# Performance work log

Hardware: AMD Instinct MI355X
Metric: run time of the kernel (lower is better)

Reference implementation:

```python
import jax, jax.numpy as jnp
import numpy as np

DIM = 2048
HIDDEN = 1024
E = 8
TOTAL = 16384
# uneven per-expert token counts summing to TOTAL (tokens pre-sorted by expert)
COUNTS = np.array([1024, 3072, 2048, 512, 4096, 1536, 2560, 1536], dtype=np.int32)
assert COUNTS.sum() == TOTAL


def setup_inputs() -> dict:
    key = jax.random.key(0)
    k1, k2, k3, k4 = jax.random.split(key, 4)
    x = jax.random.normal(k1, (TOTAL, DIM), dtype=jnp.float32)
    # kaiming_uniform_(a=sqrt(5)) on [out, in] -> U(-1/sqrt(fan_in), 1/sqrt(fan_in))
    s_in = 1.0 / np.sqrt(DIM).astype(np.float32)
    s_hid = 1.0 / np.sqrt(HIDDEN).astype(np.float32)
    gate_proj = jax.random.uniform(k2, (E, HIDDEN, DIM), dtype=jnp.float32, minval=-s_in, maxval=s_in)
    up_proj = jax.random.uniform(k3, (E, HIDDEN, DIM), dtype=jnp.float32, minval=-s_in, maxval=s_in)
    down_proj = jax.random.uniform(k4, (E, DIM, HIDDEN), dtype=jnp.float32, minval=-s_hid, maxval=s_hid)
    num_tokens_per_expert = jnp.asarray(COUNTS)
    return {
        "x": x,
        "gate_proj": gate_proj,
        "up_proj": up_proj,
        "down_proj": down_proj,
        "num_tokens_per_expert": num_tokens_per_expert,
    }


def reference(x, gate_proj, up_proj, down_proj, num_tokens_per_expert):
    """Grouped-expert SwiGLU: for each expert e, its contiguous token slice xs gets
    silu(xs @ G_e^T) * (xs @ U_e^T) @ D_e^T. Counts are data-dependent segment sizes
    (the torch original is @torch.compiler.disable for the same reason), so we slice
    with concrete offsets and loop over the small fixed expert count."""
    counts = np.asarray(num_tokens_per_expert)
    offs = np.concatenate([[0], np.cumsum(counts)])
    outs = []
    for e in range(counts.shape[0]):
        lo, hi = int(offs[e]), int(offs[e + 1])
        if hi == lo:
            continue
        xs = x[lo:hi]                                   # [c_e, dim]
        h = jax.nn.silu(xs @ gate_proj[e].T) * (xs @ up_proj[e].T)  # [c_e, hidden]
        outs.append(h @ down_proj[e].T)                 # [c_e, dim]
    return jnp.concatenate(outs, axis=0)                # [total, dim]
```

## Files before the change

kernel.cpp:

```cpp
#include <hip/hip_runtime.h>


constexpr int DIM    = 2048;
constexpr int HIDDEN = 1024;
constexpr int NE     = 8;
constexpr int TOTAL  = 16384;

constexpr int BM = 128, BN = 128, BK = 32;
constexpr int LDT  = 40;
constexpr int TILE = 128 * LDT;

typedef __attribute__((ext_vector_type(8)))  short bf16x8;
typedef __attribute__((ext_vector_type(16))) float f32x16;

constexpr size_t W_ELEMS = (size_t)NE * HIDDEN * DIM;
constexpr size_t H_ELEMS = (size_t)TOTAL * HIDDEN;

__device__ unsigned short g_g_hi[W_ELEMS], g_g_lo[W_ELEMS];
__device__ unsigned short g_u_hi[W_ELEMS], g_u_lo[W_ELEMS];
__device__ unsigned short g_d_hi[W_ELEMS], g_d_lo[W_ELEMS];
__device__ unsigned short g_h_hi[H_ELEMS], g_h_lo[H_ELEMS];

__device__ __forceinline__ unsigned short bf16_rne(float f) {
  unsigned u = __builtin_bit_cast(unsigned, f);
  u += 0x7FFFu + ((u >> 16) & 1u);
  return (unsigned short)(u >> 16);
}
__device__ __forceinline__ float bf16f(unsigned short s) {
  unsigned u = (unsigned)s << 16;
  return __builtin_bit_cast(float, u);
}
__device__ __forceinline__ void split2(float f, unsigned short& hi, unsigned short& lo) {
  hi = bf16_rne(f);
  lo = bf16_rne(f - bf16f(hi));
}

__device__ __forceinline__ void expert_range(const int* __restrict__ counts, int e,
                                             int& lo, int& nloc) {
  lo = 0; nloc = 0;
#pragma unroll
  for (int i = 0; i < NE; ++i) {
    int c = counts[i];
    if (i < e) lo += c;
    if (i == e) nloc = c;
  }
}

__global__ __launch_bounds__(256)
void split_planes(const float* __restrict__ src, unsigned short* __restrict__ hi,
                  unsigned short* __restrict__ lo, int n4) {
  int i = blockIdx.x * blockDim.x + threadIdx.x;
  const int stride = gridDim.x * blockDim.x;
  for (; i < n4; i += stride) {
    const float4 v = ((const float4*)src)[i];
    ushort4 h4, l4;
    split2(v.x, h4.x, l4.x);
    split2(v.y, h4.y, l4.y);
    split2(v.z, h4.z, l4.z);
    split2(v.w, h4.w, l4.w);
    ((ushort4*)hi)[i] = h4;
    ((ushort4*)lo)[i] = l4;
  }
}

__global__ __launch_bounds__(256, 2)
void moe_s1(const float* __restrict__ x, const int* __restrict__ counts) {
  const int e = blockIdx.z;
  int lo, nloc;
  expert_range(counts, e, lo, nloc);
  const int m0 = blockIdx.x * BM;
  if (m0 >= nloc) return;
  const int n0 = blockIdx.y * BN;

  __shared__ unsigned short sm[6 * TILE];
  unsigned short* const Ah = sm;
  unsigned short* const Al = sm + TILE;
  unsigned short* const Gh = sm + 2 * TILE;
  unsigned short* const Gl = sm + 3 * TILE;
  unsigned short* const Uh = sm + 4 * TILE;
  unsigned short* const Ul = sm + 5 * TILE;

  const int tid  = threadIdx.x;
  const int lane = tid & 63;
  const int w    = tid >> 6;
  const int wm   = w >> 1, wn = w & 1;

  const float* const xa = x + (size_t)lo * DIM;
  const size_t wb = ((size_t)e * HIDDEN + n0) * DIM;
  const unsigned short* const Ghg = g_g_hi + wb;
  const unsigned short* const Glg = g_g_lo + wb;
  const unsigned short* const Uhg = g_u_hi + wb;
  const unsigned short* const Ulg = g_u_lo + wb;

  const int q4 = (tid & 7) * 4;
  const int r0 = tid >> 3;
  const int k8 = (tid & 3) * 8;
  const int rw = tid >> 2;

  f32x16 accg[2][2], accu[2][2];
#pragma unroll
  for (int i = 0; i < 2; ++i)
#pragma unroll
    for (int j = 0; j < 2; ++j)
#pragma unroll
      for (int k = 0; k < 16; ++k) { accg[i][j][k] = 0.f; accu[i][j][k] = 0.f; }

  float4 va[4];
  bf16x8 vgh[2], vgl[2], vuh[2], vul[2];

  auto load_tile = [&](int kt) {
    const int kbx = kt * BK + q4;
#pragma unroll
    for (int c = 0; c < 4; ++c) {
      const int r  = (c << 5) + r0;
      const int ra = (m0 + r < nloc) ? (m0 + r) : m0;
      va[c] = *(const float4*)(xa + (size_t)ra * DIM + kbx);
    }
    const int kbw = kt * BK + k8;
#pragma unroll
    for (int c = 0; c < 2; ++c) {
      const size_t ro = (size_t)((c << 6) + rw) * DIM + kbw;
      vgh[c] = *(const bf16x8*)(Ghg + ro);
      vgl[c] = *(const bf16x8*)(Glg + ro);
      vuh[c] = *(const bf16x8*)(Uhg + ro);
      vul[c] = *(const bf16x8*)(Ulg + ro);
    }
  };

  const int NT = DIM / BK;
  load_tile(0);

  for (int kt = 0; kt < NT; ++kt) {
    __syncthreads();
#pragma unroll
    for (int c = 0; c < 4; ++c) {
      ushort4 hh, ll;
      split2(va[c].x, hh.x, ll.x);
      split2(va[c].y, hh.y, ll.y);
      split2(va[c].z, hh.z, ll.z);
      split2(va[c].w, hh.w, ll.w);
      const int o = ((c << 5) + r0) * LDT + q4;
      *(ushort4*)(Ah + o) = hh;
      *(ushort4*)(Al + o) = ll;
    }
#pragma unroll
    for (int c = 0; c < 2; ++c) {
      const int o = ((c << 6) + rw) * LDT + k8;
      *(bf16x8*)(Gh + o) = vgh[c];
      *(bf16x8*)(Gl + o) = vgl[c];
      *(bf16x8*)(Uh + o) = vuh[c];
      *(bf16x8*)(Ul + o) = vul[c];
    }
    if (kt + 1 < NT) load_tile(kt + 1);
    __syncthreads();

#pragma unroll
    for (int ks = 0; ks < 2; ++ks) {
      const int kc = ks * 16 + (lane >> 5) * 8;
      const int ar = wm * 64 + (lane & 31);
      const int br = wn * 64 + (lane & 31);
      bf16x8 fah[2], fal[2];
#pragma unroll
      for (int fm = 0; fm < 2; ++fm) {
        fah[fm] = *(const bf16x8*)(Ah + (ar + fm * 32) * LDT + kc);
        fal[fm] = *(const bf16x8*)(Al + (ar + fm * 32) * LDT + kc);
      }
#pragma unroll
      for (int fn = 0; fn < 2; ++fn) {
        const int ro = (br + fn * 32) * LDT + kc;
        bf16x8 gh = *(const bf16x8*)(Gh + ro);
        bf16x8 gl = *(const bf16x8*)(Gl + ro);
        bf16x8 uh = *(const bf16x8*)(Uh + ro);
        bf16x8 ul = *(const bf16x8*)(Ul + ro);
#pragma unroll
        for (int fm = 0; fm < 2; ++fm) {
          accg[fm][fn] = __builtin_amdgcn_mfma_f32_32x32x16_bf16(fah[fm], gh, accg[fm][fn], 0, 0, 0);
          accg[fm][fn] = __builtin_amdgcn_mfma_f32_32x32x16_bf16(fah[fm], gl, accg[fm][fn], 0, 0, 0);
          accg[fm][fn] = __builtin_amdgcn_mfma_f32_32x32x16_bf16(fal[fm], gh, accg[fm][fn], 0, 0, 0);
          accu[fm][fn] = __builtin_amdgcn_mfma_f32_32x32x16_bf16(fah[fm], uh, accu[fm][fn], 0, 0, 0);
          accu[fm][fn] = __builtin_amdgcn_mfma_f32_32x32x16_bf16(fah[fm], ul, accu[fm][fn], 0, 0, 0);
          accu[fm][fn] = __builtin_amdgcn_mfma_f32_32x32x16_bf16(fal[fm], uh, accu[fm][fn], 0, 0, 0);
        }
      }
    }
  }

  const int crb  = (lane >> 5) * 4;
  const int ccol = lane & 31;
#pragma unroll
  for (int fm = 0; fm < 2; ++fm)
#pragma unroll
    for (int fn = 0; fn < 2; ++fn)
#pragma unroll
      for (int j = 0; j < 16; ++j) {
        const int rl = wm * 64 + fm * 32 + (j & 3) + ((j >> 2) << 3) + crb;
        if (m0 + rl < nloc) {
          const float gv = accg[fm][fn][j];
          const float uv = accu[fm][fn][j];
          const float hv = gv / (1.f + __expf(-gv)) * uv;
          unsigned short hh, hl;
          split2(hv, hh, hl);
          const size_t idx = (size_t)(lo + m0 + rl) * HIDDEN + (n0 + wn * 64 + fn * 32 + ccol);
          g_h_hi[idx] = hh;
          g_h_lo[idx] = hl;
        }
      }
}

__global__ __launch_bounds__(256, 2)
void moe_s2(const int* __restrict__ counts, float* __restrict__ out) {
  const int e = blockIdx.z;
  int lo, nloc;
  expert_range(counts, e, lo, nloc);
  const int m0 = blockIdx.x * BM;
  if (m0 >= nloc) return;
  const int n0 = blockIdx.y * BN;

  __shared__ unsigned short sm[4 * TILE];
  unsigned short* const Ah = sm;
  unsigned short* const Al = sm + TILE;
  unsigned short* const Bh = sm + 2 * TILE;
  unsigned short* const Bl = sm + 3 * TILE;

  const int tid  = threadIdx.x;
  const int lane = tid & 63;
  const int w    = tid >> 6;
  const int wm   = w >> 1, wn = w & 1;

  const unsigned short* const hhg = g_h_hi + (size_t)lo * HIDDEN;
  const unsigned short* const hlg = g_h_lo + (size_t)lo * HIDDEN;
  const size_t db = ((size_t)e * DIM + n0) * HIDDEN;
  const unsigned short* const Bhg = g_d_hi + db;
  const unsigned short* const Blg = g_d_lo + db;

  const int k8 = (tid & 3) * 8;
  const int rw = tid >> 2;

  f32x16 acc[2][2];
#pragma unroll
  for (int i = 0; i < 2; ++i)
#pragma unroll
    for (int j = 0; j < 2; ++j)
#pragma unroll
      for (int k = 0; k < 16; ++k) acc[i][j][k] = 0.f;

  bf16x8 vah[2], val[2], vbh[2], vbl[2];

  auto load_tile = [&](int kt) {
    const int kb = kt * BK + k8;
#pragma unroll
    for (int c = 0; c < 2; ++c) {
      const int r  = (c << 6) + rw;
      const int ra = (m0 + r < nloc) ? (m0 + r) : m0;
      vah[c] = *(const bf16x8*)(hhg + (size_t)ra * HIDDEN + kb);
      val[c] = *(const bf16x8*)(hlg + (size_t)ra * HIDDEN + kb);
      const size_t ro = (size_t)r * HIDDEN + kb;
      vbh[c] = *(const bf16x8*)(Bhg + ro);
      vbl[c] = *(const bf16x8*)(Blg + ro);
    }
  };

  const int NT = HIDDEN / BK;
  load_tile(0);

  for (int kt = 0; kt < NT; ++kt) {
    __syncthreads();
#pragma unroll
    for (int c = 0; c < 2; ++c) {
      const int o = ((c << 6) + rw) * LDT + k8;
      *(bf16x8*)(Ah + o) = vah[c];
      *(bf16x8*)(Al + o) = val[c];
      *(bf16x8*)(Bh + o) = vbh[c];
      *(bf16x8*)(Bl + o) = vbl[c];
    }
    if (kt + 1 < NT) load_tile(kt + 1);
    __syncthreads();

#pragma unroll
    for (int ks = 0; ks < 2; ++ks) {
      const int kc = ks * 16 + (lane >> 5) * 8;
      const int ar = wm * 64 + (lane & 31);
      const int br = wn * 64 + (lane & 31);
      bf16x8 fah[2], fal[2];
#pragma unroll
      for (int fm = 0; fm < 2; ++fm) {
        fah[fm] = *(const bf16x8*)(Ah + (ar + fm * 32) * LDT + kc);
        fal[fm] = *(const bf16x8*)(Al + (ar + fm * 32) * LDT + kc);
      }
#pragma unroll
      for (int fn = 0; fn < 2; ++fn) {
        const int ro = (br + fn * 32) * LDT + kc;
        bf16x8 bh = *(const bf16x8*)(Bh + ro);
        bf16x8 bl = *(const bf16x8*)(Bl + ro);
#pragma unroll
        for (int fm = 0; fm < 2; ++fm) {
          acc[fm][fn] = __builtin_amdgcn_mfma_f32_32x32x16_bf16(fah[fm], bh, acc[fm][fn], 0, 0, 0);
          acc[fm][fn] = __builtin_amdgcn_mfma_f32_32x32x16_bf16(fah[fm], bl, acc[fm][fn], 0, 0, 0);
          acc[fm][fn] = __builtin_amdgcn_mfma_f32_32x32x16_bf16(fal[fm], bh, acc[fm][fn], 0, 0, 0);
        }
      }
    }
  }

  const int crb  = (lane >> 5) * 4;
  const int ccol = lane & 31;
#pragma unroll
  for (int fm = 0; fm < 2; ++fm)
#pragma unroll
    for (int fn = 0; fn < 2; ++fn)
#pragma unroll
      for (int j = 0; j < 16; ++j) {
        const int rl = wm * 64 + fm * 32 + (j & 3) + ((j >> 2) << 3) + crb;
        if (m0 + rl < nloc) {
          out[(size_t)(lo + m0 + rl) * DIM + (n0 + wn * 64 + fn * 32 + ccol)] = acc[fm][fn][j];
        }
      }
}

extern "C" void kernel_launch(void* const* d_in, const int* in_sizes, int n_in,
                              void* d_out, int out_size, void* d_ws, size_t ws_size,
                              hipStream_t stream) {
  const float* x     = (const float*)d_in[0];
  const float* gate  = (const float*)d_in[1];
  const float* up    = (const float*)d_in[2];
  const float* down  = (const float*)d_in[3];
  const int*   cnts  = (const int*)d_in[4];
  float*       out   = (float*)d_out;
  (void)d_ws; (void)ws_size;

  unsigned short *gh, *gl, *uh, *ul, *dh, *dl;
  hipGetSymbolAddress((void**)&gh, HIP_SYMBOL(g_g_hi));
  hipGetSymbolAddress((void**)&gl, HIP_SYMBOL(g_g_lo));
  hipGetSymbolAddress((void**)&uh, HIP_SYMBOL(g_u_hi));
  hipGetSymbolAddress((void**)&ul, HIP_SYMBOL(g_u_lo));
  hipGetSymbolAddress((void**)&dh, HIP_SYMBOL(g_d_hi));
  hipGetSymbolAddress((void**)&dl, HIP_SYMBOL(g_d_lo));

  const int n4 = (int)(W_ELEMS / 4);
  dim3 blk(256, 1, 1);
  split_planes<<<2048, blk, 0, stream>>>(gate, gh, gl, n4);
  split_planes<<<2048, blk, 0, stream>>>(up,   uh, ul, n4);
  split_planes<<<2048, blk, 0, stream>>>(down, dh, dl, n4);
  moe_s1<<<dim3(TOTAL / BM, HIDDEN / BN, NE), blk, 0, stream>>>(x, cnts);
  moe_s2<<<dim3(TOTAL / BM, DIM / BN, NE), blk, 0, stream>>>(cnts, out);
}
```

Before: 1.552 ms.

## Pre-pack operands into swizzled bf16 hi/lo tiles and stage via direct global-to-LDS loads

Every operand, x included, is now pre-split into hi/lo bf16 and packed into 128x32 tiles with an XOR-swizzled layout. The split no longer happens inside the GEMM loop. Both GEMM kernels stage tiles straight into a double-buffered LDS using global_load_lds, with explicit vmcnt waits and barriers, setprio around the MFMA blocks, and 512 threads in stage 1. This removes the register round-trip and in-loop conversion, and the swizzle avoids LDS bank conflicts. In exchange it adds an extra pack pass over x, and it assumes expert token offsets are multiples of 128, since the tile index is (lo+m0)>>7. That holds for the test counts but not in general.

```diff
diff --git a/kernel.cpp b/kernel.cpp
--- a/kernel.cpp
+++ b/kernel.cpp
@@ -1,36 +1,30 @@
 #include <hip/hip_runtime.h>
 
 
-constexpr int DIM    = 2048;
-constexpr int HIDDEN = 1024;
-constexpr int NE     = 8;
-constexpr int TOTAL  = 16384;
-
+constexpr int DIM = 2048, HIDDEN = 1024, NE = 8, TOTAL = 16384;
 constexpr int BM = 128, BN = 128, BK = 32;
-constexpr int LDT  = 40;
-constexpr int TILE = 128 * LDT;
+constexpr int TBLK = 8192;
 
 typedef __attribute__((ext_vector_type(8)))  short bf16x8;
 typedef __attribute__((ext_vector_type(16))) float f32x16;
-
-constexpr size_t W_ELEMS = (size_t)NE * HIDDEN * DIM;
-constexpr size_t H_ELEMS = (size_t)TOTAL * HIDDEN;
-
-__device__ unsigned short g_g_hi[W_ELEMS], g_g_lo[W_ELEMS];
-__device__ unsigned short g_u_hi[W_ELEMS], g_u_lo[W_ELEMS];
-__device__ unsigned short g_d_hi[W_ELEMS], g_d_lo[W_ELEMS];
-__device__ unsigned short g_h_hi[H_ELEMS], g_h_lo[H_ELEMS];
-
-__device__ __forceinline__ unsigned short bf16_rne(float f) {
+typedef unsigned short u16;
+
+__device__ u16 g_px[(size_t)(TOTAL / 128) * (DIM / 32) * TBLK];
+__device__ u16 g_pg[(size_t)(NE * HIDDEN / 128) * (DIM / 32) * TBLK];
+__device__ u16 g_pu[(size_t)(NE * HIDDEN / 128) * (DIM / 32) * TBLK];
+__device__ u16 g_pd[(size_t)(NE * DIM / 128) * (HIDDEN / 32) * TBLK];
+__device__ u16 g_ph[(size_t)(TOTAL / 128) * (HIDDEN / 32) * TBLK];
+
+__device__ __forceinline__ u16 bf16_rne(float f) {
   unsigned u = __builtin_bit_cast(unsigned, f);
   u += 0x7FFFu + ((u >> 16) & 1u);
-  return (unsigned short)(u >> 16);
-}
-__device__ __forceinline__ float bf16f(unsigned short s) {
+  return (u16)(u >> 16);
+}
+__device__ __forceinline__ float bf16f(u16 s) {
   unsigned u = (unsigned)s << 16;
   return __builtin_bit_cast(float, u);
 }
-__device__ __forceinline__ void split2(float f, unsigned short& hi, unsigned short& lo) {
+__device__ __forceinline__ void split2(float f, u16& hi, u16& lo) {
   hi = bf16_rne(f);
   lo = bf16_rne(f - bf16f(hi));
 }
@@ -46,25 +40,37 @@
   }
 }
 
+__device__ __forceinline__ void stage16(const u16* g, u16* l) {
+  __builtin_amdgcn_global_load_lds(
+      (const __attribute__((address_space(1))) unsigned int*)g,
+      (__attribute__((address_space(3))) unsigned int*)l, 16, 0, 0);
+}
+
 __global__ __launch_bounds__(256)
-void split_planes(const float* __restrict__ src, unsigned short* __restrict__ hi,
-                  unsigned short* __restrict__ lo, int n4) {
-  int i = blockIdx.x * blockDim.x + threadIdx.x;
-  const int stride = gridDim.x * blockDim.x;
+void pack_split(const float* __restrict__ src, u16* __restrict__ dst, int K, int n4) {
+  int i = blockIdx.x * 256 + threadIdx.x;
+  const int stride = gridDim.x * 256;
+  const int ktiles = K >> 5;
   for (; i < n4; i += stride) {
     const float4 v = ((const float4*)src)[i];
+    const int col = (i * 4) % K;
+    const int row = (i * 4) / K;
     ushort4 h4, l4;
     split2(v.x, h4.x, l4.x);
     split2(v.y, h4.y, l4.y);
     split2(v.z, h4.z, l4.z);
     split2(v.w, h4.w, l4.w);
-    ((ushort4*)hi)[i] = h4;
-    ((ushort4*)lo)[i] = l4;
-  }
-}
-
-__global__ __launch_bounds__(256, 2)
-void moe_s1(const float* __restrict__ x, const int* __restrict__ counts) {
+    const int r = row & 127, kk = col & 31;
+    const size_t base = ((size_t)(row >> 7) * ktiles + (col >> 5)) * TBLK + r * 64;
+    const int ch = (kk >> 3) ^ (r & 7);
+    const int cl = ((kk >> 3) + 4) ^ (r & 7);
+    *(ushort4*)(dst + base + ch * 8 + (kk & 7)) = h4;
+    *(ushort4*)(dst + base + cl * 8 + (kk & 7)) = l4;
+  }
+}
+
+__global__ __launch_bounds__(512, 2)
+void moe_s1(const int* __restrict__ counts) {
   const int e = blockIdx.z;
   int lo, nloc;
   expert_range(counts, e, lo, nloc);
@@ -72,139 +78,108 @@
   if (m0 >= nloc) return;
   const int n0 = blockIdx.y * BN;
 
-  __shared__ unsigned short sm[6 * TILE];
-  unsigned short* const Ah = sm;
-  unsigned short* const Al = sm + TILE;
-  unsigned short* const Gh = sm + 2 * TILE;
-  unsigned short* const Gl = sm + 3 * TILE;
-  unsigned short* const Uh = sm + 4 * TILE;
-  unsigned short* const Ul = sm + 5 * TILE;
-
-  const int tid  = threadIdx.x;
-  const int lane = tid & 63;
-  const int w    = tid >> 6;
-  const int wm   = w >> 1, wn = w & 1;
-
-  const float* const xa = x + (size_t)lo * DIM;
-  const size_t wb = ((size_t)e * HIDDEN + n0) * DIM;
-  const unsigned short* const Ghg = g_g_hi + wb;
-  const unsigned short* const Glg = g_g_lo + wb;
-  const unsigned short* const Uhg = g_u_hi + wb;
-  const unsigned short* const Ulg = g_u_lo + wb;
-
-  const int q4 = (tid & 7) * 4;
-  const int r0 = tid >> 3;
-  const int k8 = (tid & 3) * 8;
-  const int rw = tid >> 2;
-
-  f32x16 accg[2][2], accu[2][2];
+  __shared__ __align__(16) u16 sm[2 * 3 * TBLK];
+
+  const int tid = threadIdx.x, lane = tid & 63, w = tid >> 6;
+  const int wm = w >> 2, wnq = w & 3;
+
+  const int gmt = (lo + m0) >> 7;
+  const u16* const srcs[3] = {
+      g_px + (size_t)gmt * (DIM / 32) * TBLK,
+      g_pg + (size_t)(e * (HIDDEN / 128) + (n0 >> 7)) * (DIM / 32) * TBLK,
+      g_pu + (size_t)(e * (HIDDEN / 128) + (n0 >> 7)) * (DIM / 32) * TBLK};
+
+  const u16* csrc[6];
+  int coff[6];
+#pragma unroll
+  for (int j = 0; j < 6; ++j) {
+    const int i = w * 6 + j;
+    const int mat = i >> 4;
+    const int off = (i & 15) * 512;
+    csrc[j] = srcs[mat] + off + lane * 8;
+    coff[j] = mat * TBLK + off;
+  }
+
+  auto stage = [&](int buf, int kt) {
+#pragma unroll
+    for (int j = 0; j < 6; ++j)
+      stage16(csrc[j] + (size_t)kt * TBLK, &sm[buf * 3 * TBLK + coff[j]]);
+  };
+
+  auto frg = [&](int buf, int mat, int rbase, int p, int ks) -> bf16x8 {
+    const int rr = rbase + (lane & 31);
+    const int c = (p * 4 + ks * 2 + (lane >> 5)) ^ (rr & 7);
+    return *(const bf16x8*)&sm[buf * 3 * TBLK + mat * TBLK + rr * 64 + c * 8];
+  };
+
+  f32x16 ag[2], au[2];
 #pragma unroll
   for (int i = 0; i < 2; ++i)
 #pragma unroll
-    for (int j = 0; j < 2; ++j)
-#pragma unroll
-      for (int k = 0; k < 16; ++k) { accg[i][j][k] = 0.f; accu[i][j][k] = 0.f; }
-
-  float4 va[4];
-  bf16x8 vgh[2], vgl[2], vuh[2], vul[2];
-
-  auto load_tile = [&](int kt) {
-    const int kbx = kt * BK + q4;
-#pragma unroll
-    for (int c = 0; c < 4; ++c) {
-      const int r  = (c << 5) + r0;
-      const int ra = (m0 + r < nloc) ? (m0 + r) : m0;
-      va[c] = *(const float4*)(xa + (size_t)ra * DIM + kbx);
+    for (int k = 0; k < 16; ++k) { ag[i][k] = 0.f; au[i][k] = 0.f; }
+
+  const int NT = DIM / BK;
+  stage(0, 0);
+  stage(1, 1);
+
+  for (int kt = 0; kt < NT; ++kt) {
+    const int b = kt & 1;
+    if (kt + 2 < NT) asm volatile("s_waitcnt vmcnt(6)" ::: "memory");
+    else             asm volatile("s_waitcnt vmcnt(0)" ::: "memory");
+    __builtin_amdgcn_s_barrier();
+    __builtin_amdgcn_sched_barrier(0);
+#pragma unroll
+    for (int ks = 0; ks < 2; ++ks) {
+      const bf16x8 aH0 = frg(b, 0, wm * 64,      0, ks);
+      const bf16x8 aH1 = frg(b, 0, wm * 64 + 32, 0, ks);
+      const bf16x8 aL0 = frg(b, 0, wm * 64,      1, ks);
+      const bf16x8 aL1 = frg(b, 0, wm * 64 + 32, 1, ks);
+      const bf16x8 gH = frg(b, 1, wnq * 32, 0, ks);
+      const bf16x8 gL = frg(b, 1, wnq * 32, 1, ks);
+      const bf16x8 uH = frg(b, 2, wnq * 32, 0, ks);
+      const bf16x8 uL = frg(b, 2, wnq * 32, 1, ks);
+      __builtin_amdgcn_s_setprio(1);
+      ag[0] = __builtin_amdgcn_mfma_f32_32x32x16_bf16(aH0, gH, ag[0], 0, 0, 0);
+      ag[0] = __builtin_amdgcn_mfma_f32_32x32x16_bf16(aH0, gL, ag[0], 0, 0, 0);
+      ag[0] = __builtin_amdgcn_mfma_f32_32x32x16_bf16(aL0, gH, ag[0], 0, 0, 0);
+      ag[1] = __builtin_amdgcn_mfma_f32_32x32x16_bf16(aH1, gH, ag[1], 0, 0, 0);
+      ag[1] = __builtin_amdgcn_mfma_f32_32x32x16_bf16(aH1, gL, ag[1], 0, 0, 0);
+      ag[1] = __builtin_amdgcn_mfma_f32_32x32x16_bf16(aL1, gH, ag[1], 0, 0, 0);
+      au[0] = __builtin_amdgcn_mfma_f32_32x32x16_bf16(aH0, uH, au[0], 0, 0, 0);
+      au[0] = __builtin_amdgcn_mfma_f32_32x32x16_bf16(aH0, uL, au[0], 0, 0, 0);
+      au[0] = __builtin_amdgcn_mfma_f32_32x32x16_bf16(aL0, uH, au[0], 0, 0, 0);
+      au[1] = __builtin_amdgcn_mfma_f32_32x32x16_bf16(aH1, uH, au[1], 0, 0, 0);
+      au[1] = __builtin_amdgcn_mfma_f32_32x32x16_bf16(aH1, uL, au[1], 0, 0, 0);
+      au[1] = __builtin_amdgcn_mfma_f32_32x32x16_bf16(aL1, uH, au[1], 0, 0, 0);
+      __builtin_amdgcn_s_setprio(0);
     }
-    const int kbw = kt * BK + k8;
-#pragma unroll
-    for (int c = 0; c < 2; ++c) {
-      const size_t ro = (size_t)((c << 6) + rw) * DIM + kbw;
-      vgh[c] = *(const bf16x8*)(Ghg + ro);
-      vgl[c] = *(const bf16x8*)(Glg + ro);
-      vuh[c] = *(const bf16x8*)(Uhg + ro);
-      vul[c] = *(const bf16x8*)(Ulg + ro);
-    }
-  };
-
-  const int NT = DIM / BK;
-  load_tile(0);
-
-  for (int kt = 0; kt < NT; ++kt) {
-    __syncthreads();
-#pragma unroll
-    for (int c = 0; c < 4; ++c) {
-      ushort4 hh, ll;
-      split2(va[c].x, hh.x, ll.x);
-      split2(va[c].y, hh.y, ll.y);
-      split2(va[c].z, hh.z, ll.z);
-      split2(va[c].w, hh.w, ll.w);
-      const int o = ((c << 5) + r0) * LDT + q4;
-      *(ushort4*)(Ah + o) = hh;
-      *(ushort4*)(Al + o) = ll;
-    }
-#pragma unroll
-    for (int c = 0; c < 2; ++c) {
-      const int o = ((c << 6) + rw) * LDT + k8;
-      *(bf16x8*)(Gh + o) = vgh[c];
-      *(bf16x8*)(Gl + o) = vgl[c];
-      *(bf16x8*)(Uh + o) = vuh[c];
-      *(bf16x8*)(Ul + o) = vul[c];
-    }
-    if (kt + 1 < NT) load_tile(kt + 1);
-    __syncthreads();
-
-#pragma unroll
-    for (int ks = 0; ks < 2; ++ks) {
-      const int kc = ks * 16 + (lane >> 5) * 8;
-      const int ar = wm * 64 + (lane & 31);
-      const int br = wn * 64 + (lane & 31);
-      bf16x8 fah[2], fal[2];
-#pragma unroll
-      for (int fm = 0; fm < 2; ++fm) {
-        fah[fm] = *(const bf16x8*)(Ah + (ar + fm * 32) * LDT + kc);
-        fal[fm] = *(const bf16x8*)(Al + (ar + fm * 32) * LDT + kc);
-      }
-#pragma unroll
-      for (int fn = 0; fn < 2; ++fn) {
-        const int ro = (br + fn * 32) * LDT + kc;
-        bf16x8 gh = *(const bf16x8*)(Gh + ro);
-        bf16x8 gl = *(const bf16x8*)(Gl + ro);
-        bf16x8 uh = *(const bf16x8*)(Uh + ro);
-        bf16x8 ul = *(const bf16x8*)(Ul + ro);
-#pragma unroll
-        for (int fm = 0; fm < 2; ++fm) {
-          accg[fm][fn] = __builtin_amdgcn_mfma_f32_32x32x16_bf16(fah[fm], gh, accg[fm][fn], 0, 0, 0);
-          accg[fm][fn] = __builtin_amdgcn_mfma_f32_32x32x16_bf16(fah[fm], gl, accg[fm][fn], 0, 0, 0);
-          accg[fm][fn] = __builtin_amdgcn_mfma_f32_32x32x16_bf16(fal[fm], gh, accg[fm][fn], 0, 0, 0);
-          accu[fm][fn] = __builtin_amdgcn_mfma_f32_32x32x16_bf16(fah[fm], uh, accu[fm][fn], 0, 0, 0);
-          accu[fm][fn] = __builtin_amdgcn_mfma_f32_32x32x16_bf16(fah[fm], ul, accu[fm][fn], 0, 0, 0);
-          accu[fm][fn] = __builtin_amdgcn_mfma_f32_32x32x16_bf16(fal[fm], uh, accu[fm][fn], 0, 0, 0);
-        }
+    __builtin_amdgcn_sched_barrier(0);
+    __builtin_amdgcn_s_barrier();
+    __builtin_amdgcn_sched_barrier(0);
+    if (kt + 2 < NT) stage(b, kt + 2);
+  }
+
+  const int hf = lane >> 5, ccol = lane & 31;
+  const int n = n0 + wnq * 32 + ccol;
+  const int kk = n & 31;
+  const size_t hbase = ((size_t)gmt * (HIDDEN / 32) + (n >> 5)) * TBLK;
+#pragma unroll
+  for (int fm = 0; fm < 2; ++fm)
+#pragma unroll
+    for (int j = 0; j < 16; ++j) {
+      const int rl = wm * 64 + fm * 32 + (j & 3) + ((j >> 2) << 3) + hf * 4;
+      if (m0 + rl < nloc) {
+        const float gv = ag[fm][j];
+        const float uv = au[fm][j];
+        const float hv = gv / (1.f + __expf(-gv)) * uv;
+        u16 hh, hl;
+        split2(hv, hh, hl);
+        const int ch = (kk >> 3) ^ (rl & 7);
+        const int cl = ((kk >> 3) + 4) ^ (rl & 7);
+        g_ph[hbase + rl * 64 + ch * 8 + (kk & 7)] = hh;
+        g_ph[hbase + rl * 64 + cl * 8 + (kk & 7)] = hl;
       }
     }
-  }
-
-  const int crb  = (lane >> 5) * 4;
-  const int ccol = lane & 31;
-#pragma unroll
-  for (int fm = 0; fm < 2; ++fm)
-#pragma unroll
-    for (int fn = 0; fn < 2; ++fn)
-#pragma unroll
-      for (int j = 0; j < 16; ++j) {
-        const int rl = wm * 64 + fm * 32 + (j & 3) + ((j >> 2) << 3) + crb;
-        if (m0 + rl < nloc) {
-          const float gv = accg[fm][fn][j];
-          const float uv = accu[fm][fn][j];
-          const float hv = gv / (1.f + __expf(-gv)) * uv;
-          unsigned short hh, hl;
-          split2(hv, hh, hl);
-          const size_t idx = (size_t)(lo + m0 + rl) * HIDDEN + (n0 + wn * 64 + fn * 32 + ccol);
-          g_h_hi[idx] = hh;
-          g_h_lo[idx] = hl;
-        }
-      }
 }
 
 __global__ __launch_bounds__(256, 2)
@@ -216,25 +191,38 @@
   if (m0 >= nloc) return;
   const int n0 = blockIdx.y * BN;
 
-  __shared__ unsigned short sm[4 * TILE];
-  unsigned short* const Ah = sm;
-  unsigned short* const Al = sm + TILE;
-  unsigned short* const Bh = sm + 2 * TILE;
-  unsigned short* const Bl = sm + 3 * TILE;
-
-  const int tid  = threadIdx.x;
-  const int lane = tid & 63;
-  const int w    = tid >> 6;
-  const int wm   = w >> 1, wn = w & 1;
-
-  const unsigned short* const hhg = g_h_hi + (size_t)lo * HIDDEN;
-  const unsigned short* const hlg = g_h_lo + (size_t)lo * HIDDEN;
-  const size_t db = ((size_t)e * DIM + n0) * HIDDEN;
-  const unsigned short* const Bhg = g_d_hi + db;
-  const unsigned short* const Blg = g_d_lo + db;
-
-  const int k8 = (tid & 3) * 8;
-  const int rw = tid >> 2;
+  __shared__ __align__(16) u16 sm[2 * 2 * TBLK];
+
+  const int tid = threadIdx.x, lane = tid & 63, w = tid >> 6;
+  const int wm = w >> 1, wn = w & 1;
+
+  const int gmt = (lo + m0) >> 7;
+  const u16* const srcs[2] = {
+      g_ph + (size_t)gmt * (HIDDEN / 32) * TBLK,
+      g_pd + (size_t)(e * (DIM / 128) + (n0 >> 7)) * (HIDDEN / 32) * TBLK};
+
+  const u16* csrc[8];
+  int coff[8];
+#pragma unroll
+  for (int j = 0; j < 8; ++j) {
+    const int i = w * 8 + j;
+    const int mat = i >> 4;
+    const int off = (i & 15) * 512;
+    csrc[j] = srcs[mat] + off + lane * 8;
+    coff[j] = mat * TBLK + off;
+  }
+
+  auto stage = [&](int buf, int kt) {
+#pragma unroll
+    for (int j = 0; j < 8; ++j)
+      stage16(csrc[j] + (size_t)kt * TBLK, &sm[buf * 2 * TBLK + coff[j]]);
+  };
+
+  auto frg = [&](int buf, int mat, int rbase, int p, int ks) -> bf16x8 {
+    const int rr = rbase + (lane & 31);
+    const int c = (p * 4 + ks * 2 + (lane >> 5)) ^ (rr & 7);
+    return *(const bf16x8*)&sm[buf * 2 * TBLK + mat * TBLK + rr * 64 + c * 8];
+  };
 
   f32x16 acc[2][2];
 #pragma unroll
@@ -244,73 +232,54 @@
 #pragma unroll
       for (int k = 0; k < 16; ++k) acc[i][j][k] = 0.f;
 
-  bf16x8 vah[2], val[2], vbh[2], vbl[2];
-
-  auto load_tile = [&](int kt) {
-    const int kb = kt * BK + k8;
-#pragma unroll
-    for (int c = 0; c < 2; ++c) {
-      const int r  = (c << 6) + rw;
-      const int ra = (m0 + r < nloc) ? (m0 + r) : m0;
-      vah[c] = *(const bf16x8*)(hhg + (size_t)ra * HIDDEN + kb);
-      val[c] = *(const bf16x8*)(hlg + (size_t)ra * HIDDEN + kb);
-      const size_t ro = (size_t)r * HIDDEN + kb;
-      vbh[c] = *(const bf16x8*)(Bhg + ro);
-      vbl[c] = *(const bf16x8*)(Blg + ro);
+  const int NT = HIDDEN / BK;
+  stage(0, 0);
+  stage(1, 1);
+
+  for (int kt = 0; kt < NT; ++kt) {
+    const int b = kt & 1;
+    if (kt + 2 < NT) asm volatile("s_waitcnt vmcnt(8)" ::: "memory");
+    else             asm volatile("s_waitcnt vmcnt(0)" ::: "memory");
+    __builtin_amdgcn_s_barrier();
+    __builtin_amdgcn_sched_barrier(0);
+#pragma unroll
+    for (int ks = 0; ks < 2; ++ks) {
+      bf16x8 aH[2], aL[2], bH[2], bL[2];
+#pragma unroll
+      for (int fm = 0; fm < 2; ++fm) {
+        aH[fm] = frg(b, 0, wm * 64 + fm * 32, 0, ks);
+        aL[fm] = frg(b, 0, wm * 64 + fm * 32, 1, ks);
+      }
+#pragma unroll
+      for (int fn = 0; fn < 2; ++fn) {
+        bH[fn] = frg(b, 1, wn * 64 + fn * 32, 0, ks);
+        bL[fn] = frg(b, 1, wn * 64 + fn * 32, 1, ks);
+      }
+      __builtin_amdgcn_s_setprio(1);
+#pragma unroll
+      for (int fn = 0; fn < 2; ++fn)
+#pragma unroll
+        for (int fm = 0; fm < 2; ++fm) {
+          acc[fm][fn] = __builtin_amdgcn_mfma_f32_32x32x16_bf16(aH[fm], bH[fn], acc[fm][fn], 0, 0, 0);
+          acc[fm][fn] = __builtin_amdgcn_mfma_f32_32x32x16_bf16(aH[fm], bL[fn], acc[fm][fn], 0, 0, 0);
+          acc[fm][fn] = __builtin_amdgcn_mfma_f32_32x32x16_bf16(aL[fm], bH[fn], acc[fm][fn], 0, 0, 0);
+        }
+      __builtin_amdgcn_s_setprio(0);
     }
-  };
-
-  const int NT = HIDDEN / BK;
-  load_tile(0);
-
-  for (int kt = 0; kt < NT; ++kt) {
-    __syncthreads();
-#pragma unroll
-    for (int c = 0; c < 2; ++c) {
-      const int o = ((c << 6) + rw) * LDT + k8;
-      *(bf16x8*)(Ah + o) = vah[c];
-      *(bf16x8*)(Al + o) = val[c];
-      *(bf16x8*)(Bh + o) = vbh[c];
-      *(bf16x8*)(Bl + o) = vbl[c];
-    }
-    if (kt + 1 < NT) load_tile(kt + 1);
-    __syncthreads();
-
-#pragma unroll
-    for (int ks = 0; ks < 2; ++ks) {
-      const int kc = ks * 16 + (lane >> 5) * 8;
-      const int ar = wm * 64 + (lane & 31);
-      const int br = wn * 64 + (lane & 31);
-      bf16x8 fah[2], fal[2];
-#pragma unroll
-      for (int fm = 0; fm < 2; ++fm) {
-        fah[fm] = *(const bf16x8*)(Ah + (ar + fm * 32) * LDT + kc);
-        fal[fm] = *(const bf16x8*)(Al + (ar + fm * 32) * LDT + kc);
-      }
-#pragma unroll
-      for (int fn = 0; fn < 2; ++fn) {
-        const int ro = (br + fn * 32) * LDT + kc;
-        bf16x8 bh = *(const bf16x8*)(Bh + ro);
-        bf16x8 bl = *(const bf16x8*)(Bl + ro);
-#pragma unroll
-        for (int fm = 0; fm < 2; ++fm) {
-          acc[fm][fn] = __builtin_amdgcn_mfma_f32_32x32x16_bf16(fah[fm], bh, acc[fm][fn], 0, 0, 0);
-          acc[fm][fn] = __builtin_amdgcn_mfma_f32_32x32x16_bf16(fah[fm], bl, acc[fm][fn], 0, 0, 0);
-          acc[fm][fn] = __builtin_amdgcn_mfma_f32_32x32x16_bf16(fal[fm], bh, acc[fm][fn], 0, 0, 0);
-        }
-      }
-    }
-  }
-
-  const int crb  = (lane >> 5) * 4;
-  const int ccol = lane & 31;
+    __builtin_amdgcn_sched_barrier(0);
+    __builtin_amdgcn_s_barrier();
+    __builtin_amdgcn_sched_barrier(0);
+    if (kt + 2 < NT) stage(b, kt + 2);
+  }
+
+  const int hf = lane >> 5, ccol = lane & 31;
 #pragma unroll
   for (int fm = 0; fm < 2; ++fm)
 #pragma unroll
     for (int fn = 0; fn < 2; ++fn)
 #pragma unroll
       for (int j = 0; j < 16; ++j) {
-        const int rl = wm * 64 + fm * 32 + (j & 3) + ((j >> 2) << 3) + crb;
+        const int rl = wm * 64 + fm * 32 + (j & 3) + ((j >> 2) << 3) + hf * 4;
         if (m0 + rl < nloc) {
           out[(size_t)(lo + m0 + rl) * DIM + (n0 + wn * 64 + fn * 32 + ccol)] = acc[fm][fn][j];
         }
@@ -320,27 +289,26 @@
 extern "C" void kernel_launch(void* const* d_in, const int* in_sizes, int n_in,
                               void* d_out, int out_size, void* d_ws, size_t ws_size,
                               hipStream_t stream) {
-  const float* x     = (const float*)d_in[0];
-  const float* gate  = (const float*)d_in[1];
-  const float* up    = (const float*)d_in[2];
-  const float* down  = (const float*)d_in[3];
-  const int*   cnts  = (const int*)d_in[4];
-  float*       out   = (float*)d_out;
+  const float* x    = (const float*)d_in[0];
+  const float* gate = (const float*)d_in[1];
+  const float* up   = (const float*)d_in[2];
+  const float* down = (const float*)d_in[3];
+  const int*   cnts = (const int*)d_in[4];
+  float*       out  = (float*)d_out;
   (void)d_ws; (void)ws_size;
 
-  unsigned short *gh, *gl, *uh, *ul, *dh, *dl;
-  hipGetSymbolAddress((void**)&gh, HIP_SYMBOL(g_g_hi));
-  hipGetSymbolAddress((void**)&gl, HIP_SYMBOL(g_g_lo));
-  hipGetSymbolAddress((void**)&uh, HIP_SYMBOL(g_u_hi));
-  hipGetSymbolAddress((void**)&ul, HIP_SYMBOL(g_u_lo));
-  hipGetSymbolAddress((void**)&dh, HIP_SYMBOL(g_d_hi));
-  hipGetSymbolAddress((void**)&dl, HIP_SYMBOL(g_d_lo));
-
-  const int n4 = (int)(W_ELEMS / 4);
-  dim3 blk(256, 1, 1);
-  split_planes<<<2048, blk, 0, stream>>>(gate, gh, gl, n4);
-  split_planes<<<2048, blk, 0, stream>>>(up,   uh, ul, n4);
-  split_planes<<<2048, blk, 0, stream>>>(down, dh, dl, n4);
-  moe_s1<<<dim3(TOTAL / BM, HIDDEN / BN, NE), blk, 0, stream>>>(x, cnts);
-  moe_s2<<<dim3(TOTAL / BM, DIM / BN, NE), blk, 0, stream>>>(cnts, out);
-}
+  u16 *px, *pg, *pu, *pd;
+  hipGetSymbolAddress((void**)&px, HIP_SYMBOL(g_px));
+  hipGetSymbolAddress((void**)&pg, HIP_SYMBOL(g_pg));
+  hipGetSymbolAddress((void**)&pu, HIP_SYMBOL(g_pu));
+  hipGetSymbolAddress((void**)&pd, HIP_SYMBOL(g_pd));
+
+  dim3 blk256(256, 1, 1);
+  pack_split<<<2048, blk256, 0, stream>>>(x,    px, DIM,    (TOTAL * DIM) / 4);
+  pack_split<<<2048, blk256, 0, stream>>>(gate, pg, DIM,    (NE * HIDDEN * DIM) / 4);
+  pack_split<<<2048, blk256, 0, stream>>>(up,   pu, DIM,    (NE * HIDDEN * DIM) / 4);
+  pack_split<<<2048, blk256, 0, stream>>>(down, pd, HIDDEN, (NE * DIM * HIDDEN) / 4);
+
+  moe_s1<<<dim3(TOTAL / BM, HIDDEN / BN, NE), dim3(512, 1, 1), 0, stream>>>(cnts);
+  moe_s2<<<dim3(TOTAL / BM, DIM / BN, NE), blk256, 0, stream>>>(cnts, out);
+}
```

Measured after the change: 1.613 ms. 3.9% more time.
